# Optimization experiments

Hardware: AMD Instinct MI355X
Metric: run time of the kernel (lower is better)

Reference implementation:

```python
import jax, jax.numpy as jnp
import numpy as np

EMBED = 768
DIM = 800          # embed + 32 gender features
IN_C = 1024
GRID = 32          # img_size // patch_size(=1)
LN_EPS = 1e-5      # torch nn.LayerNorm default


def setup_inputs() -> dict:
    key = jax.random.key(0)
    ks = jax.random.split(key, 8)
    B = 32
    x = jax.random.normal(ks[0], (B, IN_C, GRID, GRID), dtype=jnp.float32)
    gender_encode = jax.random.normal(ks[1], (B, 32), dtype=jnp.float32)
    # PatchEmbed 1x1 conv (acts as per-pixel linear) + LayerNorm params
    conv_w = jax.random.normal(ks[2], (EMBED, IN_C), dtype=jnp.float32) * (IN_C ** -0.5)
    conv_b = jnp.zeros((EMBED,), dtype=jnp.float32)
    ln_g = jnp.ones((EMBED,), dtype=jnp.float32)
    ln_b = jnp.zeros((EMBED,), dtype=jnp.float32)
    cls_token = jax.random.normal(ks[3], (1, 1, EMBED), dtype=jnp.float32) * 0.02
    # Attention qkv linear (bias=True); proj is never used in the forward path
    qkv_w = jax.random.normal(ks[4], (3 * DIM, DIM), dtype=jnp.float32) * (DIM ** -0.5)
    qkv_b = jnp.zeros((3 * DIM,), dtype=jnp.float32)
    return {
        "x": x, "gender_encode": gender_encode,
        "conv_w": conv_w, "conv_b": conv_b,
        "ln_g": ln_g, "ln_b": ln_b,
        "cls_token": cls_token,
        "qkv_w": qkv_w, "qkv_b": qkv_b,
    }


def _forward(x, gender_encode, conv_w, conv_b, ln_g, ln_b, cls_token, qkv_w, qkv_b):
    B = x.shape[0]
    # PatchEmbed: 1x1 conv stride 1 == per-pixel linear; flatten(2).transpose(1,2)
    p = jnp.einsum('bchw,oc->bhwo', x, conv_w) + conv_b        # [B,32,32,768]
    p = p.reshape(B, GRID * GRID, EMBED)                        # [B,1024,768]
    mu = jnp.mean(p, axis=-1, keepdims=True)
    var = jnp.mean((p - mu) ** 2, axis=-1, keepdims=True)
    p = (p - mu) * jax.lax.rsqrt(var + LN_EPS) * ln_g + ln_b
    # prepend cls token, concat broadcast gender features
    cls = jnp.broadcast_to(cls_token, (B, 1, EMBED))
    t = jnp.concatenate([cls, p], axis=1)                       # [B,1025,768]
    g = jnp.broadcast_to(gender_encode[:, None, :], (B, t.shape[1], 32))
    t = jnp.concatenate([t, g], axis=2)                         # [B,1025,800]
    # Attention (note: self.norm / proj / v are unused in the original forward)
    qkv = t @ qkv_w.T + qkv_b                                   # [B,1025,2400]
    q = qkv[..., 0:DIM]
    k = qkv[..., DIM:2 * DIM]
    scale = DIM ** -0.5
    # only the cls-query row is ever used -> compute just that row
    scores = jnp.einsum('bc,bnc->bn', q[:, 0], k) * scale       # [B,1025]
    attn_cls = jax.nn.softmax(scores[:, 1:], axis=-1)           # [B,1024]
    return attn_cls.reshape(B, 1, GRID, GRID)


def reference(x, gender_encode, conv_w, conv_b, ln_g, ln_b, cls_token, qkv_w, qkv_b):
    return _forward(x, gender_encode, conv_w, conv_b, ln_g, ln_b, cls_token, qkv_w, qkv_b)
```

## Files before the change

### kernel.cpp

```cpp
#include <hip/hip_runtime.h>
#include <hip/hip_bf16.h>

#define EMBED 768
#define DIMQ  800
#define INC   1024
#define NPIX  1024

typedef __bf16 bf16_t;
typedef __bf16 bf16x8 __attribute__((ext_vector_type(8)));
typedef __bf16 bf16x2 __attribute__((ext_vector_type(2)));
typedef float  f32x4  __attribute__((ext_vector_type(4)));

#define GLD_LDS(gp, lp) __builtin_amdgcn_global_load_lds( \
    (const __attribute__((address_space(1))) void*)(gp),  \
    (__attribute__((address_space(3))) void*)(lp), 16, 0, 0)

__global__ __launch_bounds__(256)
void k_prep(const float* __restrict__ x, bf16_t* __restrict__ xT,
            const float* __restrict__ w, bf16_t* __restrict__ cw,
            const float* __restrict__ qkv_w, const float* __restrict__ qkv_b,
            const float* __restrict__ cls, const float* __restrict__ gender,
            float* __restrict__ q0b) {
    __shared__ __align__(16) unsigned int tile[64 * 36];
    const int bi = blockIdx.x;
    const int t  = threadIdx.x;
    if (bi < 8192) {
        const int b  = bi >> 8;
        const int k0 = ((bi >> 4) & 15) * 64;
        const int m0 = (bi & 15) * 64;
        const int m_l = t & 63;
        const int wv  = t >> 6;
        const float* src = x + ((size_t)(b * 1024 + k0 + wv * 16) * 1024) + m0 + m_l;
        bf16x2* trow = (bf16x2*)tile;
#pragma unroll
        for (int i = 0; i < 8; ++i) {
            float a0 = src[(size_t)(2 * i) * 1024];
            float a1 = src[(size_t)(2 * i + 1) * 1024];
            bf16x2 p; p[0] = (bf16_t)a0; p[1] = (bf16_t)a1;
            trow[m_l * 36 + wv * 8 + i] = p;
        }
        __syncthreads();
        const int m_r = t >> 2;
        bf16_t* drow = xT + ((size_t)(b * 1024 + m0 + m_r) * 1024) + k0;
#pragma unroll
        for (int rep = 0; rep < 2; ++rep) {
            int j = (t & 3) + rep * 4;
            bf16x8 v = *(const bf16x8*)&tile[m_r * 36 + j * 4];
            int slot = j ^ (m_r & 7);
            *(bf16x8*)(drow + slot * 8) = v;
        }
    } else if (bi < 8392) {
        const int wv = t >> 6, tl = t & 63;
        const int i = (bi - 8192) * 4 + wv;
        const float* row = qkv_w + (size_t)i * DIMQ;
        float ps = 0.f;
        for (int j = tl; j < EMBED; j += 64) ps += row[j] * cls[j];
#pragma unroll
        for (int off = 1; off < 64; off <<= 1) ps += __shfl_xor(ps, off, 64);
        if (tl < 32) {
            float g = 0.f;
#pragma unroll
            for (int j = 0; j < 32; ++j) g += row[EMBED + j] * gender[tl * 32 + j];
            q0b[tl * DIMQ + i] = ps + g + qkv_b[i];
        }
    } else {
        const int i = (bi - 8392) * 256 + t;
        const int n = i >> 10, k = i & 1023;
        const int s = (k >> 3) & 7;
        const int src_k = (k & ~63) | (((s ^ (n & 7)) & 7) << 3) | (k & 7);
        cw[i] = (bf16_t)w[(size_t)n * 1024 + src_k];
    }
}

__global__ __launch_bounds__(256)
void k_u(const float* __restrict__ qkv_w, const float* __restrict__ q0b,
         const float* __restrict__ ln_g, float* __restrict__ u) {
    __shared__ float q0s[DIMQ];
    __shared__ float sh[8][33];
    int t = threadIdx.x;
    int b  = blockIdx.x / 24;
    int j0 = (blockIdx.x % 24) * 32;
    for (int i = t; i < DIMQ; i += 256) q0s[i] = q0b[b * DIMQ + i];
    __syncthreads();
    int j_l = t & 31, os = t >> 5;
    const float* wk = qkv_w + (size_t)DIMQ * DIMQ;
    const float* wp = wk + (size_t)(os * 100) * DIMQ + j0 + j_l;
    float acc = 0.f;
#pragma unroll 4
    for (int i = 0; i < 100; ++i) acc += wp[(size_t)i * DIMQ] * q0s[os * 100 + i];
    sh[os][j_l] = acc;
    __syncthreads();
    if (t < 32) {
        float s = 0.f;
#pragma unroll
        for (int o = 0; o < 8; ++o) s += sh[o][t];
        u[b * EMBED + j0 + t] = s * ln_g[j0 + t];
    }
}

__global__ __launch_bounds__(256, 3)
void k_main(const bf16_t* __restrict__ xT, const bf16_t* __restrict__ cw,
            const float* __restrict__ conv_b, const float* __restrict__ u,
            float* __restrict__ partial) {
    __shared__ __align__(1024) unsigned char smem[32768 + 3072];

    const int tid = threadIdx.x;
    const int bi = blockIdx.x;
    const int x8 = bi & 7;
    const int s  = bi >> 3;
    const int nt = s % 6;
    const int mt = (s / 6) * 8 + x8;
    const int b  = mt >> 3;
    const int gm = mt * 128;
    const int gn = nt * 128;

    const int wv = tid >> 6;
    const int l  = tid & 63;
    const int lr = l >> 3;
    const int lc = l & 7;

    const int lane = l;
    const int col  = lane & 15;
    const int quad = lane >> 4;
    const int wm   = (wv >> 1) * 64;
    const int wn   = (wv & 1) * 64;

    bf16_t* A = (bf16_t*)smem;
    bf16_t* B = (bf16_t*)(smem + 16384);

    f32x4 C[4][4] = {};

    for (int kt = 0; kt < 16; ++kt) {
        const int ko = kt * 64;
#pragma unroll
        for (int p = 0; p < 4; ++p) {
            const int r = p * 32 + wv * 8 + lr;
            GLD_LDS(xT + (size_t)(gm + r) * 1024 + ko + lc * 8, A + (p * 32 + wv * 8) * 64);
            GLD_LDS(cw + (size_t)(gn + r) * 1024 + ko + lc * 8, B + (p * 32 + wv * 8) * 64);
        }
        __syncthreads();
#pragma unroll
        for (int ks = 0; ks < 2; ++ks) {
            bf16x8 af[4], bg[4];
#pragma unroll
            for (int mi = 0; mi < 4; ++mi) {
                const int r  = wm + mi * 16 + col;
                const int ph = (ks * 4 + quad) ^ (r & 7);
                af[mi] = *(const bf16x8*)(A + r * 64 + ph * 8);
            }
#pragma unroll
            for (int ni = 0; ni < 4; ++ni) {
                const int r  = wn + ni * 16 + col;
                const int ph = (ks * 4 + quad) ^ (r & 7);
                bg[ni] = *(const bf16x8*)(B + r * 64 + ph * 8);
            }
#pragma unroll
            for (int mi = 0; mi < 4; ++mi)
#pragma unroll
                for (int ni = 0; ni < 4; ++ni)
                    C[mi][ni] = __builtin_amdgcn_mfma_f32_16x16x32_bf16(af[mi], bg[ni], C[mi][ni], 0, 0, 0);
        }
        __syncthreads();
    }

    float cb[4], uv[4];
#pragma unroll
    for (int ni = 0; ni < 4; ++ni) {
        const int og = gn + wn + ni * 16 + col;
        cb[ni] = conv_b[og];
        uv[ni] = u[b * EMBED + og];
    }
    float* part = (float*)(smem + 32768);
#pragma unroll
    for (int mi = 0; mi < 4; ++mi)
#pragma unroll
        for (int r = 0; r < 4; ++r) {
            float a = 0.f, sq = 0.f, d = 0.f;
#pragma unroll
            for (int ni = 0; ni < 4; ++ni) {
                float v = C[mi][ni][r] + cb[ni];
                a += v; sq += v * v; d += v * uv[ni];
            }
#pragma unroll
            for (int off = 1; off < 16; off <<= 1) {
                a  += __shfl_xor(a, off, 64);
                sq += __shfl_xor(sq, off, 64);
                d  += __shfl_xor(d, off, 64);
            }
            if (col == 0) {
                const int row = wm + mi * 16 + quad * 4 + r;
                float* pp = part + ((wv & 1) * 128 + row) * 3;
                pp[0] = a; pp[1] = sq; pp[2] = d;
            }
        }
    __syncthreads();
    if (tid < 128) {
        const float* p0 = part + tid * 3;
        const float* p1 = part + (128 + tid) * 3;
        const size_t pix = (size_t)gm + tid;
        partial[(size_t)(0 * 6 + nt) * 32768 + pix] = p0[0] + p1[0];
        partial[(size_t)(1 * 6 + nt) * 32768 + pix] = p0[1] + p1[1];
        partial[(size_t)(2 * 6 + nt) * 32768 + pix] = p0[2] + p1[2];
    }
}

__global__ __launch_bounds__(1024)
void k_final(const float* __restrict__ partial, const float* __restrict__ u,
             float* __restrict__ out) {
    __shared__ float red[16];
    __shared__ float bc[3];
    const int b = blockIdx.x, t = threadIdx.x;
    const int lane = t & 63, wid = t >> 6;

    float pu = (t < EMBED) ? u[b * EMBED + t] : 0.f;
#pragma unroll
    for (int off = 1; off < 64; off <<= 1) pu += __shfl_xor(pu, off, 64);
    if (lane == 0) red[wid] = pu;
    __syncthreads();
    if (t == 0) { float s = 0.f; for (int i = 0; i < 16; ++i) s += red[i]; bc[0] = s; }
    __syncthreads();
    const float Su = bc[0];

    const size_t m = (size_t)b * 1024 + t;
    float S1 = 0.f, S2 = 0.f, S3 = 0.f;
#pragma unroll
    for (int nt = 0; nt < 6; ++nt) {
        S1 += partial[(size_t)(0 * 6 + nt) * 32768 + m];
        S2 += partial[(size_t)(1 * 6 + nt) * 32768 + m];
        S3 += partial[(size_t)(2 * 6 + nt) * 32768 + m];
    }
    const float mu  = S1 * (1.f / 768.f);
    const float var = S2 * (1.f / 768.f) - mu * mu;
    const float sc  = 0.035355339059327376f * (S3 - mu * Su) * rsqrtf(var + 1e-5f);

    float mx = sc;
#pragma unroll
    for (int off = 1; off < 64; off <<= 1) mx = fmaxf(mx, __shfl_xor(mx, off, 64));
    if (lane == 0) red[wid] = mx;
    __syncthreads();
    if (t == 0) { float mm = -1e30f; for (int i = 0; i < 16; ++i) mm = fmaxf(mm, red[i]); bc[1] = mm; }
    __syncthreads();
    const float e = __expf(sc - bc[1]);
    float ss = e;
#pragma unroll
    for (int off = 1; off < 64; off <<= 1) ss += __shfl_xor(ss, off, 64);
    __syncthreads();
    if (lane == 0) red[wid] = ss;
    __syncthreads();
    if (t == 0) { float s = 0.f; for (int i = 0; i < 16; ++i) s += red[i]; bc[2] = s; }
    __syncthreads();
    out[m] = e / bc[2];
}

extern "C" void kernel_launch(void* const* d_in, const int* in_sizes, int n_in,
                              void* d_out, int out_size, void* d_ws, size_t ws_size,
                              hipStream_t stream) {
    const float* x      = (const float*)d_in[0];
    const float* gender = (const float*)d_in[1];
    const float* conv_w = (const float*)d_in[2];
    const float* conv_b = (const float*)d_in[3];
    const float* ln_g   = (const float*)d_in[4];
    const float* cls    = (const float*)d_in[6];
    const float* qkv_w  = (const float*)d_in[7];
    const float* qkv_b  = (const float*)d_in[8];
    float* out = (float*)d_out;

    char* ws = (char*)d_ws;
    bf16_t* cw      = (bf16_t*)ws;
    float*  q0b     = (float*)(ws + 1572864);
    float*  u       = (float*)(ws + 1675264);
    float*  partial = (float*)(ws + 1773568);
    bf16_t* xT      = (bf16_t*)(ws + 4132864);

    hipLaunchKernelGGL(k_prep,  dim3(11464), dim3(256),  0, stream,
                       x, xT, conv_w, cw, qkv_w, qkv_b, cls, gender, q0b);
    hipLaunchKernelGGL(k_u,     dim3(768),   dim3(256),  0, stream, qkv_w, q0b, ln_g, u);
    hipLaunchKernelGGL(k_main,  dim3(1536),  dim3(256),  0, stream, xT, cw, conv_b, u, partial);
    hipLaunchKernelGGL(k_final, dim3(32),    dim3(1024), 0, stream, partial, u, out);
}
```

Before: 295.7 us.

## Enlarge GEMM tiles to 256x256 with double-buffered LDS pipeline

Reworks the main conv-GEMM kernel to use 256x256 output tiles with 512 threads, a double-buffered 128KB dynamic LDS pipeline that prefetches two K-steps ahead, and s_setprio/barrier interleaving around MFMA groups. The aim is to raise arithmetic intensity and hide global-to-LDS load latency. The number of N tiles per pixel drops from 6 to 3, so the partial-sum layout and the final reduction are adjusted to match. The trade-offs are fewer blocks (384) on a 256-CU device, which can leave the tail unbalanced, and more accumulator registers per thread.

```diff
diff --git a/kernel.cpp b/kernel.cpp
--- a/kernel.cpp
+++ b/kernel.cpp
@@ -98,70 +98,104 @@
     }
 }
 
-__global__ __launch_bounds__(256, 3)
+__global__ __launch_bounds__(512, 2)
 void k_main(const bf16_t* __restrict__ xT, const bf16_t* __restrict__ cw,
             const float* __restrict__ conv_b, const float* __restrict__ u,
             float* __restrict__ partial) {
-    __shared__ __align__(1024) unsigned char smem[32768 + 3072];
+    extern __shared__ unsigned char smem[];
 
     const int tid = threadIdx.x;
     const int bi = blockIdx.x;
     const int x8 = bi & 7;
     const int s  = bi >> 3;
-    const int nt = s % 6;
-    const int mt = (s / 6) * 8 + x8;
-    const int b  = mt >> 3;
-    const int gm = mt * 128;
-    const int gn = nt * 128;
+    const int nt = s % 3;
+    const int mt = (s / 3) * 8 + x8;
+    const int b  = mt >> 2;
+    const int gm = mt * 256;
+    const int gn = nt * 256;
 
     const int wv = tid >> 6;
     const int l  = tid & 63;
     const int lr = l >> 3;
     const int lc = l & 7;
 
-    const int lane = l;
-    const int col  = lane & 15;
-    const int quad = lane >> 4;
-    const int wm   = (wv >> 1) * 64;
-    const int wn   = (wv & 1) * 64;
-
-    bf16_t* A = (bf16_t*)smem;
-    bf16_t* B = (bf16_t*)(smem + 16384);
-
-    f32x4 C[4][4] = {};
-
-    for (int kt = 0; kt < 16; ++kt) {
-        const int ko = kt * 64;
-#pragma unroll
-        for (int p = 0; p < 4; ++p) {
-            const int r = p * 32 + wv * 8 + lr;
-            GLD_LDS(xT + (size_t)(gm + r) * 1024 + ko + lc * 8, A + (p * 32 + wv * 8) * 64);
-            GLD_LDS(cw + (size_t)(gn + r) * 1024 + ko + lc * 8, B + (p * 32 + wv * 8) * 64);
-        }
-        __syncthreads();
+    const int col  = l & 15;
+    const int quad = l >> 4;
+    const int wm   = (wv >> 2) * 128;
+    const int wn   = (wv & 3) * 64;
+
+    bf16_t* A0 = (bf16_t*)(smem);
+    bf16_t* B0 = (bf16_t*)(smem + 32768);
+    bf16_t* A1 = (bf16_t*)(smem + 65536);
+    bf16_t* B1 = (bf16_t*)(smem + 98304);
+
+    const bf16_t* asrc = xT + (size_t)(gm + lr) * 1024 + lc * 8;
+    const bf16_t* bsrc = cw + (size_t)(gn + lr) * 1024 + lc * 8;
+
+    f32x4 C[8][4] = {};
+
+#define ISSUE(tt, Ab, Bb) do {                                              \
+        const size_t ko_ = (size_t)(tt) * 64;                               \
+        _Pragma("unroll")                                                   \
+        for (int j = 0; j < 4; ++j) {                                       \
+            const int rg = j * 64 + wv * 8;                                 \
+            GLD_LDS(asrc + (size_t)rg * 1024 + ko_, (Ab) + rg * 64);        \
+            GLD_LDS(bsrc + (size_t)rg * 1024 + ko_, (Bb) + rg * 64);        \
+        }                                                                   \
+    } while (0)
+
+    ISSUE(0, A0, B0);
+    ISSUE(1, A1, B1);
+    asm volatile("s_waitcnt vmcnt(8)" ::: "memory");
+    asm volatile("s_barrier" ::: "memory");
+
+    for (int t = 0; t < 16; ++t) {
+        bf16_t* Ab = (t & 1) ? A1 : A0;
+        bf16_t* Bb = (t & 1) ? B1 : B0;
 #pragma unroll
         for (int ks = 0; ks < 2; ++ks) {
-            bf16x8 af[4], bg[4];
-#pragma unroll
-            for (int mi = 0; mi < 4; ++mi) {
-                const int r  = wm + mi * 16 + col;
-                const int ph = (ks * 4 + quad) ^ (r & 7);
-                af[mi] = *(const bf16x8*)(A + r * 64 + ph * 8);
-            }
+            bf16x8 bg[4];
 #pragma unroll
             for (int ni = 0; ni < 4; ++ni) {
                 const int r  = wn + ni * 16 + col;
                 const int ph = (ks * 4 + quad) ^ (r & 7);
-                bg[ni] = *(const bf16x8*)(B + r * 64 + ph * 8);
-            }
-#pragma unroll
-            for (int mi = 0; mi < 4; ++mi)
-#pragma unroll
-                for (int ni = 0; ni < 4; ++ni)
-                    C[mi][ni] = __builtin_amdgcn_mfma_f32_16x16x32_bf16(af[mi], bg[ni], C[mi][ni], 0, 0, 0);
-        }
-        __syncthreads();
-    }
+                bg[ni] = *(const bf16x8*)(Bb + r * 64 + ph * 8);
+            }
+#pragma unroll
+            for (int g = 0; g < 2; ++g) {
+                bf16x8 af[4];
+#pragma unroll
+                for (int mi = 0; mi < 4; ++mi) {
+                    const int r  = wm + (g * 4 + mi) * 16 + col;
+                    const int ph = (ks * 4 + quad) ^ (r & 7);
+                    af[mi] = *(const bf16x8*)(Ab + r * 64 + ph * 8);
+                }
+                __builtin_amdgcn_s_barrier();
+                __builtin_amdgcn_s_setprio(1);
+#pragma unroll
+                for (int mi = 0; mi < 4; ++mi)
+#pragma unroll
+                    for (int ni = 0; ni < 4; ++ni)
+                        C[g * 4 + mi][ni] = __builtin_amdgcn_mfma_f32_16x16x32_bf16(
+                            af[mi], bg[ni], C[g * 4 + mi][ni], 0, 0, 0);
+                __builtin_amdgcn_s_setprio(0);
+                __builtin_amdgcn_s_barrier();
+            }
+        }
+        if (t < 15) {
+            asm volatile("s_barrier" ::: "memory");
+            if (t + 2 < 16) {
+                bf16_t* An = (t & 1) ? A1 : A0;
+                bf16_t* Bn = (t & 1) ? B1 : B0;
+                ISSUE(t + 2, An, Bn);
+                asm volatile("s_waitcnt vmcnt(8)" ::: "memory");
+            } else {
+                asm volatile("s_waitcnt vmcnt(0)" ::: "memory");
+            }
+            asm volatile("s_barrier" ::: "memory");
+        }
+    }
+#undef ISSUE
 
     float cb[4], uv[4];
 #pragma unroll
@@ -170,9 +204,10 @@
         cb[ni] = conv_b[og];
         uv[ni] = u[b * EMBED + og];
     }
-    float* part = (float*)(smem + 32768);
-#pragma unroll
-    for (int mi = 0; mi < 4; ++mi)
+    float* part = (float*)smem;
+    asm volatile("s_barrier" ::: "memory");
+#pragma unroll
+    for (int mi = 0; mi < 8; ++mi)
 #pragma unroll
         for (int r = 0; r < 4; ++r) {
             float a = 0.f, sq = 0.f, d = 0.f;
@@ -189,18 +224,22 @@
             }
             if (col == 0) {
                 const int row = wm + mi * 16 + quad * 4 + r;
-                float* pp = part + ((wv & 1) * 128 + row) * 3;
+                float* pp = part + ((wv & 3) * 256 + row) * 3;
                 pp[0] = a; pp[1] = sq; pp[2] = d;
             }
         }
     __syncthreads();
-    if (tid < 128) {
-        const float* p0 = part + tid * 3;
-        const float* p1 = part + (128 + tid) * 3;
+    if (tid < 256) {
+        float s1 = 0.f, s2 = 0.f, s3 = 0.f;
+#pragma unroll
+        for (int g2 = 0; g2 < 4; ++g2) {
+            const float* pp = part + (g2 * 256 + tid) * 3;
+            s1 += pp[0]; s2 += pp[1]; s3 += pp[2];
+        }
         const size_t pix = (size_t)gm + tid;
-        partial[(size_t)(0 * 6 + nt) * 32768 + pix] = p0[0] + p1[0];
-        partial[(size_t)(1 * 6 + nt) * 32768 + pix] = p0[1] + p1[1];
-        partial[(size_t)(2 * 6 + nt) * 32768 + pix] = p0[2] + p1[2];
+        partial[(size_t)(0 * 3 + nt) * 32768 + pix] = s1;
+        partial[(size_t)(1 * 3 + nt) * 32768 + pix] = s2;
+        partial[(size_t)(2 * 3 + nt) * 32768 + pix] = s3;
     }
 }
 
@@ -224,10 +263,10 @@
     const size_t m = (size_t)b * 1024 + t;
     float S1 = 0.f, S2 = 0.f, S3 = 0.f;
 #pragma unroll
-    for (int nt = 0; nt < 6; ++nt) {
-        S1 += partial[(size_t)(0 * 6 + nt) * 32768 + m];
-        S2 += partial[(size_t)(1 * 6 + nt) * 32768 + m];
-        S3 += partial[(size_t)(2 * 6 + nt) * 32768 + m];
+    for (int nt = 0; nt < 3; ++nt) {
+        S1 += partial[(size_t)(0 * 3 + nt) * 32768 + m];
+        S2 += partial[(size_t)(1 * 3 + nt) * 32768 + m];
+        S3 += partial[(size_t)(2 * 3 + nt) * 32768 + m];
     }
     const float mu  = S1 * (1.f / 768.f);
     const float var = S2 * (1.f / 768.f) - mu * mu;
@@ -272,9 +311,16 @@
     float*  partial = (float*)(ws + 1773568);
     bf16_t* xT      = (bf16_t*)(ws + 4132864);
 
+    static bool s_attr = false;
+    if (!s_attr) {
+        hipFuncSetAttribute(reinterpret_cast<const void*>(k_main),
+                            hipFuncAttributeMaxDynamicSharedMemorySize, 131072);
+        s_attr = true;
+    }
+
     hipLaunchKernelGGL(k_prep,  dim3(11464), dim3(256),  0, stream,
                        x, xT, conv_w, cw, qkv_w, qkv_b, cls, gender, q0b);
     hipLaunchKernelGGL(k_u,     dim3(768),   dim3(256),  0, stream, qkv_w, q0b, ln_g, u);
-    hipLaunchKernelGGL(k_main,  dim3(1536),  dim3(256),  0, stream, xT, cw, conv_b, u, partial);
+    hipLaunchKernelGGL(k_main,  dim3(384),   dim3(512),  131072, stream, xT, cw, conv_b, u, partial);
     hipLaunchKernelGGL(k_final, dim3(32),    dim3(1024), 0, stream, partial, u, out);
 }
```

After: 322.4 us. 9.0% more time.

## Fuse x transpose and bf16 conversion into main GEMM A-tile loads

Applied to the files above, without the earlier changes.

Drops the separate prep pass that transposed x into a bf16 xT workspace. The main GEMM now loads fp32 x directly with register loads, converts to bf16 and writes the swizzled A tile into LDS. This avoids writing and rereading a 64MB intermediate. In exchange, each x tile is read as fp32 once per N-tile (six times), A loading is no longer async global_load_lds, and the loop gains register pressure and conversion work.

```diff
diff --git a/kernel.cpp b/kernel.cpp
--- a/kernel.cpp
+++ b/kernel.cpp
@@ -16,42 +16,15 @@
     (__attribute__((address_space(3))) void*)(lp), 16, 0, 0)
 
 __global__ __launch_bounds__(256)
-void k_prep(const float* __restrict__ x, bf16_t* __restrict__ xT,
-            const float* __restrict__ w, bf16_t* __restrict__ cw,
+void k_prep(const float* __restrict__ w, bf16_t* __restrict__ cw,
             const float* __restrict__ qkv_w, const float* __restrict__ qkv_b,
             const float* __restrict__ cls, const float* __restrict__ gender,
             float* __restrict__ q0b) {
-    __shared__ __align__(16) unsigned int tile[64 * 36];
     const int bi = blockIdx.x;
     const int t  = threadIdx.x;
-    if (bi < 8192) {
-        const int b  = bi >> 8;
-        const int k0 = ((bi >> 4) & 15) * 64;
-        const int m0 = (bi & 15) * 64;
-        const int m_l = t & 63;
-        const int wv  = t >> 6;
-        const float* src = x + ((size_t)(b * 1024 + k0 + wv * 16) * 1024) + m0 + m_l;
-        bf16x2* trow = (bf16x2*)tile;
-#pragma unroll
-        for (int i = 0; i < 8; ++i) {
-            float a0 = src[(size_t)(2 * i) * 1024];
-            float a1 = src[(size_t)(2 * i + 1) * 1024];
-            bf16x2 p; p[0] = (bf16_t)a0; p[1] = (bf16_t)a1;
-            trow[m_l * 36 + wv * 8 + i] = p;
-        }
-        __syncthreads();
-        const int m_r = t >> 2;
-        bf16_t* drow = xT + ((size_t)(b * 1024 + m0 + m_r) * 1024) + k0;
-#pragma unroll
-        for (int rep = 0; rep < 2; ++rep) {
-            int j = (t & 3) + rep * 4;
-            bf16x8 v = *(const bf16x8*)&tile[m_r * 36 + j * 4];
-            int slot = j ^ (m_r & 7);
-            *(bf16x8*)(drow + slot * 8) = v;
-        }
-    } else if (bi < 8392) {
+    if (bi < 200) {
         const int wv = t >> 6, tl = t & 63;
-        const int i = (bi - 8192) * 4 + wv;
+        const int i = bi * 4 + wv;
         const float* row = qkv_w + (size_t)i * DIMQ;
         float ps = 0.f;
         for (int j = tl; j < EMBED; j += 64) ps += row[j] * cls[j];
@@ -64,7 +37,7 @@
             q0b[tl * DIMQ + i] = ps + g + qkv_b[i];
         }
     } else {
-        const int i = (bi - 8392) * 256 + t;
+        const int i = (bi - 200) * 256 + t;
         const int n = i >> 10, k = i & 1023;
         const int s = (k >> 3) & 7;
         const int src_k = (k & ~63) | (((s ^ (n & 7)) & 7) << 3) | (k & 7);
@@ -99,7 +72,7 @@
 }
 
 __global__ __launch_bounds__(256, 3)
-void k_main(const bf16_t* __restrict__ xT, const bf16_t* __restrict__ cw,
+void k_main(const float* __restrict__ x, const bf16_t* __restrict__ cw,
             const float* __restrict__ conv_b, const float* __restrict__ u,
             float* __restrict__ partial) {
     __shared__ __align__(1024) unsigned char smem[32768 + 3072];
@@ -112,6 +85,7 @@
     const int mt = (s / 6) * 8 + x8;
     const int b  = mt >> 3;
     const int gm = mt * 128;
+    const int gmm = gm & 1023;
     const int gn = nt * 128;
 
     const int wv = tid >> 6;
@@ -128,6 +102,9 @@
     bf16_t* A = (bf16_t*)smem;
     bf16_t* B = (bf16_t*)(smem + 16384);
 
+    const int m4 = (tid >> 3) * 4;
+    const float* xsrc = x + ((size_t)(b * 1024 + (tid & 7) * 8) * 1024) + gmm + m4;
+
     f32x4 C[4][4] = {};
 
     for (int kt = 0; kt < 16; ++kt) {
@@ -135,8 +112,20 @@
 #pragma unroll
         for (int p = 0; p < 4; ++p) {
             const int r = p * 32 + wv * 8 + lr;
-            GLD_LDS(xT + (size_t)(gm + r) * 1024 + ko + lc * 8, A + (p * 32 + wv * 8) * 64);
             GLD_LDS(cw + (size_t)(gn + r) * 1024 + ko + lc * 8, B + (p * 32 + wv * 8) * 64);
+        }
+        f32x4 f4[8];
+#pragma unroll
+        for (int kk = 0; kk < 8; ++kk)
+            f4[kk] = *(const f32x4*)(xsrc + (size_t)(ko + kk) * 1024);
+#pragma unroll
+        for (int mm = 0; mm < 4; ++mm) {
+            bf16x8 w8;
+#pragma unroll
+            for (int kk = 0; kk < 8; ++kk) w8[kk] = (bf16_t)f4[kk][mm];
+            const int r  = m4 + mm;
+            const int ss = (tid & 7) ^ (r & 7);
+            *(bf16x8*)(A + r * 64 + ss * 8) = w8;
         }
         __syncthreads();
 #pragma unroll
@@ -270,11 +259,10 @@
     float*  q0b     = (float*)(ws + 1572864);
     float*  u       = (float*)(ws + 1675264);
     float*  partial = (float*)(ws + 1773568);
-    bf16_t* xT      = (bf16_t*)(ws + 4132864);
-
-    hipLaunchKernelGGL(k_prep,  dim3(11464), dim3(256),  0, stream,
-                       x, xT, conv_w, cw, qkv_w, qkv_b, cls, gender, q0b);
+
+    hipLaunchKernelGGL(k_prep,  dim3(3272),  dim3(256),  0, stream,
+                       conv_w, cw, qkv_w, qkv_b, cls, gender, q0b);
     hipLaunchKernelGGL(k_u,     dim3(768),   dim3(256),  0, stream, qkv_w, q0b, ln_g, u);
-    hipLaunchKernelGGL(k_main,  dim3(1536),  dim3(256),  0, stream, xT, cw, conv_b, u, partial);
+    hipLaunchKernelGGL(k_main,  dim3(1536),  dim3(256),  0, stream, x, cw, conv_b, u, partial);
     hipLaunchKernelGGL(k_final, dim3(32),    dim3(1024), 0, stream, partial, u, out);
 }
```

Measured after the change: 314.5 us. +6.4%, slower.
